# Optimization experiments

Measured on AMD Instinct MI355X. Metric: run time of the kernel, lower is better.

The kernel has to match this reference:

```python
import jax, jax.numpy as jnp
import numpy as np

N_NODES = 50000
N_EDGES = 800000
HIDDEN = 128
N_REL = 64
NUM_HEADS = 8
HEAD_DIM = HIDDEN // NUM_HEADS


def setup_inputs() -> dict:
    key = jax.random.key(0)
    ks = jax.random.split(key, 20)
    s = 0.05
    inp = {
        "x": jax.random.normal(ks[0], (N_NODES, HIDDEN), dtype=jnp.float32),
        "timestamps": jax.random.uniform(ks[1], (N_NODES,), dtype=jnp.float32),
        "src": jax.random.randint(ks[2], (N_EDGES,), 0, N_NODES),
        "dst": jax.random.randint(ks[3], (N_EDGES,), 0, N_NODES),
        "edge_type": jax.random.randint(ks[4], (N_EDGES,), 0, N_REL),
        "edge_time": jax.random.uniform(ks[5], (N_EDGES,), dtype=jnp.float32),
        # parameters (torch Linear stored as [in, out] so we use x @ W + b)
        "rel_table": jax.random.normal(ks[6], (N_REL, HIDDEN), dtype=jnp.float32) * s,
        "Wq": jax.random.normal(ks[7], (HIDDEN, HIDDEN), dtype=jnp.float32) * s,
        "bq": jnp.zeros((HIDDEN,), dtype=jnp.float32),
        "Wk": jax.random.normal(ks[8], (HIDDEN, HIDDEN), dtype=jnp.float32) * s,
        "bk": jnp.zeros((HIDDEN,), dtype=jnp.float32),
        "Wv": jax.random.normal(ks[9], (HIDDEN, HIDDEN), dtype=jnp.float32) * s,
        "bv": jnp.zeros((HIDDEN,), dtype=jnp.float32),
        "W1": jax.random.normal(ks[10], (2 * HIDDEN + 1, HIDDEN), dtype=jnp.float32) * s,
        "b1": jnp.zeros((HIDDEN,), dtype=jnp.float32),
        "W2": jax.random.normal(ks[11], (HIDDEN, 1), dtype=jnp.float32) * s,
        "b2": jnp.zeros((1,), dtype=jnp.float32),
        "time_coeff": jnp.array(1.0, dtype=jnp.float32),
    }
    return inp


def reference(x, timestamps, src, dst, edge_type, edge_time, rel_table,
              Wq, bq, Wk, bk, Wv, bv, W1, b1, W2, b2, time_coeff):
    N = x.shape[0]
    # temporal gating
    delta_t = (timestamps[dst] - edge_time) / (jnp.abs(time_coeff) + 1e-9)  # [E]
    time_mask = jax.nn.sigmoid(delta_t)[:, None]                            # [E,1]
    rel_emb = rel_table[edge_type] * time_mask                              # [E,H]
    src_emb = x[src]                                                        # [E,H]
    # dynamic edge weights: MLP([src_emb, rel_emb, time_mask]) -> sigmoid
    weight_input = jnp.concatenate([src_emb, rel_emb, time_mask], axis=-1)  # [E,2H+1]
    h = jax.nn.relu(weight_input @ W1 + b1)
    dynamic_weights = jax.nn.sigmoid(h @ W2 + b2)                           # [E,1]
    message = src_emb * rel_emb * dynamic_weights                           # [E,H]
    # multi-head edge attention keyed by dst
    q = (x[dst] @ Wq + bq).reshape(-1, NUM_HEADS, HEAD_DIM)
    k = (message @ Wk + bk).reshape(-1, NUM_HEADS, HEAD_DIM)
    v = (message @ Wv + bv).reshape(-1, NUM_HEADS, HEAD_DIM)
    scores = (q * k).sum(-1) / (HEAD_DIM ** 0.5)                            # [E,heads]
    # scatter softmax over edges grouped by dst
    seg_max = jax.ops.segment_max(scores, dst, num_segments=N)              # [N,heads]
    e = jnp.exp(scores - seg_max[dst])
    denom = jax.ops.segment_sum(e, dst, num_segments=N)
    attn = e / denom[dst]                                                   # [E,heads]
    out = jax.ops.segment_sum(v * attn[..., None], dst, num_segments=N)     # [N,heads,hd]
    return out.reshape(N, NUM_HEADS * HEAD_DIM)
```

## Files before the change

### kernel.cpp

```cpp
#include <hip/hip_runtime.h>

typedef __bf16 v8bf __attribute__((ext_vector_type(8)));
typedef __bf16 v4bf __attribute__((ext_vector_type(4)));
typedef float  v4f  __attribute__((ext_vector_type(4)));

#define MFMA16x16x32 __builtin_amdgcn_mfma_f32_16x16x32_bf16

#define HIDDEN 128
#define NHEADS 8

__global__ __launch_bounds__(512) void prep_all(
    const float* __restrict__ rel, const float* __restrict__ W1,
    const float* __restrict__ Wk, const float* __restrict__ Wv,
    const float* __restrict__ W2, const int* __restrict__ dst,
    int* __restrict__ count,
    __bf16* __restrict__ mlppre, __bf16* __restrict__ relbf,
    __bf16* __restrict__ wswz, __bf16* __restrict__ w2bf,
    float* __restrict__ outz,
    const float* __restrict__ x, const float* __restrict__ Wq,
    const float* __restrict__ bq, const float* __restrict__ b1,
    __bf16* __restrict__ qbf, __bf16* __restrict__ hpre, __bf16* __restrict__ xbf,
    int N, int E, int hb, int zb, int nz4)
{
  __shared__ __bf16 X[32][136];
  const int b = blockIdx.x;
  if (b < 64) {
    __shared__ float rrow[128];
    const int j = threadIdx.x;
    if (j < 128) rrow[j] = rel[b*HIDDEN + j];
    __syncthreads();
    if (j < 128) {
      float acc = W1[256*HIDDEN + j];
      #pragma unroll 4
      for (int k=0;k<128;k++) acc += rrow[k]*W1[(128+k)*HIDDEN + j];
      mlppre[b*HIDDEN + j] = (__bf16)acc;
      relbf [b*HIDDEN + j] = (__bf16)rrow[j];
    }
    return;
  }
  if (b < 72) {
    int f = (b - 64)*512 + threadIdx.x;
    if (f < 128) w2bf[f] = (__bf16)W2[f];
    if (f >= 2*8*4*64) return;
    int lane = f & 63, kk = (f>>6)&3, c = (f>>8)&7, mat = f>>11;
    const float* W = mat ? Wv : Wk;
    int qq = lane>>4, nn = lane&15;
    v8bf o;
    #pragma unroll
    for (int j=0;j<8;j++) o[j] = (__bf16)W[(kk*32 + qq*8 + j)*HIDDEN + c*16 + nn];
    *(v8bf*)(wswz + (long)f*8) = o;
    return;
  }
  if (b < 72 + hb) {
    long i = (long)(b - 72)*512 + threadIdx.x;
    long e4 = i*4;
    if (e4 + 3 < E) {
      int4 d = *(const int4*)(dst + e4);
      atomicAdd(&count[d.x], 1);
      atomicAdd(&count[d.y], 1);
      atomicAdd(&count[d.z], 1);
      atomicAdd(&count[d.w], 1);
    } else {
      for (long e = e4; e < E; e++) atomicAdd(&count[dst[e]], 1);
    }
    return;
  }
  if (b < 72 + hb + zb) {
    int idx = (b - 72 - hb)*512 + threadIdx.x;
    if (idx < nz4) ((float4*)outz)[idx] = make_float4(0.f,0.f,0.f,0.f);
    return;
  }
  const int pb = b - (72 + hb + zb), npb = gridDim.x - (72 + hb + zb);
  const int tid = threadIdx.x;
  const int w = tid >> 6, l = tid & 63, qd = l >> 4, ln = l & 15;
  const int col = w*16 + ln;

  v8bf BQ[4], BH[4];
  #pragma unroll
  for (int kk=0; kk<4; kk++) {
    v8bf f, g;
    #pragma unroll
    for (int j=0;j<8;j++){
      f[j] = (__bf16)Wq[(kk*32 + qd*8 + j)*HIDDEN + col];
      g[j] = (__bf16)W1[(kk*32 + qd*8 + j)*HIDDEN + col];
    }
    BQ[kk] = f; BH[kk] = g;
  }
  const float bqv = bq[col], b1v = b1[col];

  const int s = tid >> 4, c8 = (tid & 15)*8;
  for (int n0 = pb*32; n0 < N; n0 += npb*32) {
    __syncthreads();
    int n = n0 + s;
    v8bf xv;
    if (n < N) {
      const float4* xp = (const float4*)(x + (long)n*HIDDEN + c8);
      float4 a = xp[0], b2_ = xp[1];
      xv[0]=(__bf16)a.x; xv[1]=(__bf16)a.y; xv[2]=(__bf16)a.z; xv[3]=(__bf16)a.w;
      xv[4]=(__bf16)b2_.x; xv[5]=(__bf16)b2_.y; xv[6]=(__bf16)b2_.z; xv[7]=(__bf16)b2_.w;
      *(v8bf*)(xbf + (long)n*HIDDEN + c8) = xv;
    } else {
      #pragma unroll
      for (int j=0;j<8;j++) xv[j] = (__bf16)0.f;
    }
    *(v8bf*)&X[s][c8] = xv;
    __syncthreads();

    v4f q0={0.f,0.f,0.f,0.f}, q1={0.f,0.f,0.f,0.f};
    v4f h0={0.f,0.f,0.f,0.f}, h1={0.f,0.f,0.f,0.f};
    #pragma unroll
    for (int kk=0;kk<4;kk++) {
      v8bf a0 = *(const v8bf*)&X[ln][kk*32 + qd*8];
      v8bf a1 = *(const v8bf*)&X[16+ln][kk*32 + qd*8];
      q0 = MFMA16x16x32(a0, BQ[kk], q0, 0,0,0);
      q1 = MFMA16x16x32(a1, BQ[kk], q1, 0,0,0);
      h0 = MFMA16x16x32(a0, BH[kk], h0, 0,0,0);
      h1 = MFMA16x16x32(a1, BH[kk], h1, 0,0,0);
    }
    #pragma unroll
    for (int r=0;r<4;r++) {
      int n_o = n0 + qd*4 + r;
      if (n_o < N) {
        qbf [(long)n_o*HIDDEN + col] = (__bf16)(q0[r] + bqv);
        hpre[(long)n_o*HIDDEN + col] = (__bf16)(h0[r] + b1v);
      }
      int n2 = n0 + 16 + qd*4 + r;
      if (n2 < N) {
        qbf [(long)n2*HIDDEN + col] = (__bf16)(q1[r] + bqv);
        hpre[(long)n2*HIDDEN + col] = (__bf16)(h1[r] + b1v);
      }
    }
  }
}

__global__ __launch_bounds__(1024) void scan_kernel(const int* __restrict__ count,
    int* __restrict__ base, int N)
{
  __shared__ int ssum[1024];
  const int t = threadIdx.x;
  const int chunk = ((N + 4095) >> 12) << 2;
  const int lo = t*chunk, hi = min(lo + chunk, N);
  int s = 0;
  int i = lo;
  for (; i + 3 < hi; i += 4) {
    int4 v = *(const int4*)(count + i);
    s += v.x + v.y + v.z + v.w;
  }
  for (; i < hi; i++) s += count[i];
  ssum[t] = s;
  __syncthreads();
  #pragma unroll
  for (int ofs = 1; ofs < 1024; ofs <<= 1) {
    int v = (t >= ofs) ? ssum[t - ofs] : 0;
    __syncthreads();
    ssum[t] += v;
    __syncthreads();
  }
  int run = (t == 0) ? 0 : ssum[t-1];
  i = lo;
  for (; i + 3 < hi; i += 4) {
    int4 c = *(const int4*)(count + i);
    int4 o;
    o.x = run; o.y = run + c.x; o.z = o.y + c.y; o.w = o.z + c.z;
    *(int4*)(base + i) = o;
    run = o.w + c.w;
  }
  for (; i < hi; i++) { base[i] = run; run += count[i]; }
}

__global__ __launch_bounds__(512) void scat_dw(
    const int* __restrict__ src, const int* __restrict__ dstp,
    const int* __restrict__ etyp, const float* __restrict__ etime,
    const float* __restrict__ ts, const float* __restrict__ tc,
    const __bf16* __restrict__ hpre, const __bf16* __restrict__ mlppre,
    const __bf16* __restrict__ w2bf, const float* __restrict__ b2,
    const int* __restrict__ base, int* __restrict__ cursor,
    int4* __restrict__ meta4, int E)
{
  const int tid = threadIdx.x;
  const int wid = tid >> 6, l = tid & 63;
  const long e0 = ((long)blockIdx.x*8 + wid)*4;
  const int ei = l >> 4, lc = l & 15;

  int s_=0, d_=0, ty_=0; float et_=0.f, tsd_=0.f;
  if (l < 4 && e0 + l < E) {
    long e = e0 + l;
    s_ = src[e]; d_ = dstp[e]; ty_ = etyp[e]; et_ = etime[e]; tsd_ = ts[d_];
  }
  const int sE  = __shfl(s_, ei);
  const int dE  = __shfl(d_, ei);
  const int tyE = __shfl(ty_, ei);
  const float etE  = __shfl(et_, ei);
  const float tsdE = __shfl(tsd_, ei);

  const float invtc = 1.0f / (fabsf(tc[0]) + 1e-9f);
  const float dt = (tsdE - etE) * invtc;
  const float tm = 1.0f/(1.0f + __expf(-dt));

  const v8bf w2v = *(const v8bf*)(w2bf + lc*8);
  v8bf av = *(const v8bf*)(hpre  + (long)sE *HIDDEN + lc*8);
  v8bf bp = *(const v8bf*)(mlppre+ (long)tyE*HIDDEN + lc*8);

  float z = 0.f;
  #pragma unroll
  for (int j=0;j<8;j++){
    float pj = (float)av[j] + tm*(float)bp[j];
    z += fmaxf(pj, 0.f)*(float)w2v[j];
  }
  z += __shfl_xor(z,1); z += __shfl_xor(z,2);
  z += __shfl_xor(z,4); z += __shfl_xor(z,8);

  if (lc == 0 && e0 + ei < E) {
    float dw = 1.0f/(1.0f + __expf(-(z + b2[0])));
    int p = base[dE] + atomicAdd(&cursor[dE], 1);
    meta4[p] = make_int4(sE, dE, tyE, __float_as_int(tm * dw));
  }
}

__global__ __launch_bounds__(512, 4) void edge_fused5(
    const int4* __restrict__ meta4,
    const __bf16* __restrict__ xbf, const __bf16* __restrict__ qbf,
    const __bf16* __restrict__ relbf, const __bf16* __restrict__ wswz,
    const float* __restrict__ bk, const float* __restrict__ bv,
    float* __restrict__ out, float* __restrict__ denom, int E, int ntiles)
{
  __shared__ __align__(16) __bf16 MSG[2][4096];

  const int tid = threadIdx.x;
  const int wid = tid >> 6, l = tid & 63, qd = l >> 4, ln = l & 15;
  const int eIdx = wid*4 + qd;

  v8bf bkf[4], bvf[4];
  #pragma unroll
  for (int kk=0;kk<4;kk++){
    bkf[kk] = *(const v8bf*)(wswz +         wid*2048 + kk*512 + (size_t)l*8);
    bvf[kk] = *(const v8bf*)(wswz + 16384 + wid*2048 + kk*512 + (size_t)l*8);
  }
  const float bkc = bk[wid*16 + ln];
  const float bvc = bv[wid*16 + ln];

  const int g = gridDim.x;
  int t = blockIdx.x;
  if (t >= ntiles) return;

  int4 mt = make_int4(0, -1, 0, 0);
  { int e = t*32 + l; if (l < 32 && e < E) mt = meta4[e]; }
  int tn = t + g;
  int4 mtn = make_int4(0, -1, 0, 0);
  if (tn < ntiles) { int e = tn*32 + l; if (l < 32 && e < E) mtn = meta4[e]; }

  float sME = __int_as_float(__shfl(mt.w, eIdx));
  v8bf sv, rv;
  {
    int srcE = __shfl(mt.x, eIdx);
    int tyE  = __shfl(mt.z, eIdx);
    sv = *(const v8bf*)(xbf   + (long)srcE*HIDDEN + ln*8);
    rv = *(const v8bf*)(relbf + (long)tyE *HIDDEN + ln*8);
  }
  int dC[2][4];
  #pragma unroll
  for (int b=0;b<2;b++)
    #pragma unroll
    for (int r=0;r<4;r++) dC[b][r] = __shfl(mt.y, b*16 + qd*4 + r);
  float qA[2][4];
  #pragma unroll
  for (int b=0;b<2;b++)
    #pragma unroll
    for (int r=0;r<4;r++){
      int d = dC[b][r];
      qA[b][r] = (float)qbf[(long)(d<0?0:d)*HIDDEN + wid*16 + ln];
    }

  int p = 0;
  while (true) {
    const int d_m = mt.y;

    int dprev = __shfl(d_m, (l>0)?(l-1):0);
    int flag = (l < 32) && ((l==0) || (d_m != dprev));
    unsigned long long segmask = __ballot(flag);

    const int t2 = tn + g;
    int4 mt2 = make_int4(0, -1, 0, 0);
    if (t2 < ntiles) { int e = t2*32 + l; if (l < 32 && e < E) mt2 = meta4[e]; }

    const float sMN = __int_as_float(__shfl(mtn.w, eIdx));
    const int srcN = __shfl(mtn.x, eIdx);
    const int tyN  = __shfl(mtn.z, eIdx);
    int dN[2][4];
    #pragma unroll
    for (int b=0;b<2;b++)
      #pragma unroll
      for (int r=0;r<4;r++) dN[b][r] = __shfl(mtn.y, b*16 + qd*4 + r);

    {
      char* wbase = (char*)&MSG[p][0] + eIdx*256;
      const int sw = (eIdx & 7) << 4;
      v8bf m;
      #pragma unroll
      for (int j=0;j<8;j++) m[j] = (__bf16)((float)sv[j]*(float)rv[j]*sME);
      *(v8bf*)(wbase + ((ln*16) ^ sw)) = m;
    }

    sv = *(const v8bf*)(xbf   + (long)srcN*HIDDEN + ln*8);
    rv = *(const v8bf*)(relbf + (long)tyN *HIDDEN + ln*8);

    float qB[2][4];
    #pragma unroll
    for (int b=0;b<2;b++)
      #pragma unroll
      for (int r=0;r<4;r++){
        int d = dN[b][r];
        qB[b][r] = (float)qbf[(long)(d<0?0:d)*HIDDEN + wid*16 + ln];
      }

    asm volatile("s_waitcnt lgkmcnt(0)" ::: "memory");
    __builtin_amdgcn_s_barrier();
    __builtin_amdgcn_sched_barrier(0);

    const char* rb = (const char*)&MSG[p][0];
    v4f aK[2], aV[2];
    __builtin_amdgcn_s_setprio(1);
    #pragma unroll
    for (int b=0;b<2;b++){
      const int rrow = b*16 + ln;
      const char* abase = rb + rrow*256;
      const int asw = (rrow & 7) << 4;
      v4f k_ = {0.f,0.f,0.f,0.f}, v_ = {0.f,0.f,0.f,0.f};
      #pragma unroll
      for (int kk=0;kk<4;kk++){
        v8bf a = *(const v8bf*)(abase + ((kk*64 + qd*16) ^ asw));
        k_ = MFMA16x16x32(a, bkf[kk], k_, 0,0,0);
        v_ = MFMA16x16x32(a, bvf[kk], v_, 0,0,0);
      }
      aK[b] = k_; aV[b] = v_;
    }
    __builtin_amdgcn_s_setprio(0);

    float sc[2][4];
    #pragma unroll
    for (int b=0;b<2;b++)
      #pragma unroll
      for (int r=0;r<4;r++) sc[b][r] = (aK[b][r] + bkc)*qA[b][r];
    #pragma unroll
    for (int m=1;m<16;m<<=1){
      #pragma unroll
      for (int b=0;b<2;b++)
        #pragma unroll
        for (int r=0;r<4;r++) sc[b][r] += __shfl_xor(sc[b][r], m);
    }
    float ee[2][4], wv[2][4];
    #pragma unroll
    for (int b=0;b<2;b++)
      #pragma unroll
      for (int r=0;r<4;r++){
        float e_ = __expf(sc[b][r]*0.25f);
        ee[b][r] = e_;
        wv[b][r] = e_*(aV[b][r] + bvc);
      }

    unsigned long long mm = segmask;
    while (mm){
      int s0 = __ffsll((long long)mm) - 1;
      mm &= mm - 1;
      int s1 = mm ? (__ffsll((long long)mm) - 1) : 32;
      int dseg = __shfl(d_m, s0);
      if (dseg < 0) continue;
      float a0 = 0.f, dn0 = 0.f;
      #pragma unroll
      for (int b=0;b<2;b++)
        #pragma unroll
        for (int r=0;r<4;r++){
          int rw = b*16 + qd*4 + r;
          bool in = (rw >= s0) && (rw < s1);
          a0  += in ? wv[b][r] : 0.f;
          dn0 += in ? ee[b][r] : 0.f;
        }
      a0  += __shfl_xor(a0,16);  a0  += __shfl_xor(a0,32);
      dn0 += __shfl_xor(dn0,16); dn0 += __shfl_xor(dn0,32);
      if (l < 16) atomicAdd(&out[(long)dseg*HIDDEN + wid*16 + ln], a0);
      if (l == 0) atomicAdd(&denom[(long)dseg*NHEADS + wid], dn0);
    }

    if (tn >= ntiles) break;
    t = tn; tn = t2; mt = mtn; mtn = mt2; sME = sMN;
    #pragma unroll
    for (int b=0;b<2;b++)
      #pragma unroll
      for (int r=0;r<4;r++){
        dC[b][r] = dN[b][r];
        qA[b][r] = qB[b][r];
      }
    p ^= 1;
  }
}

__global__ __launch_bounds__(512) void q_kernel(const float* __restrict__ x,
    const float* __restrict__ Wq, const float* __restrict__ bq,
    float* __restrict__ q, int N)
{
  __shared__ __bf16 X[32][136];
  const int tid = threadIdx.x;
  const int w = tid >> 6, l = tid & 63, qd = l >> 4, ln = l & 15;
  const int col = w*16 + ln;
  v8bf B[4];
  #pragma unroll
  for (int kk=0; kk<4; kk++) {
    v8bf f;
    #pragma unroll
    for (int j=0;j<8;j++) f[j] = (__bf16)Wq[(kk*32 + qd*8 + j)*HIDDEN + col];
    B[kk] = f;
  }
  const float bqv = bq[col];
  const int s = tid >> 4, c8 = (tid & 15)*8;
  for (int n0 = blockIdx.x*32; n0 < N; n0 += gridDim.x*32) {
    __syncthreads();
    int n = n0 + s;
    v8bf xv;
    if (n < N) {
      const float4* xp = (const float4*)(x + (long)n*HIDDEN + c8);
      float4 a = xp[0], b = xp[1];
      xv[0]=(__bf16)a.x; xv[1]=(__bf16)a.y; xv[2]=(__bf16)a.z; xv[3]=(__bf16)a.w;
      xv[4]=(__bf16)b.x; xv[5]=(__bf16)b.y; xv[6]=(__bf16)b.z; xv[7]=(__bf16)b.w;
    } else {
      #pragma unroll
      for (int j=0;j<8;j++) xv[j] = (__bf16)0.f;
    }
    *(v8bf*)&X[s][c8] = xv;
    __syncthreads();
    v4f acc0 = {0.f,0.f,0.f,0.f}, acc1 = {0.f,0.f,0.f,0.f};
    #pragma unroll
    for (int kk=0;kk<4;kk++) {
      v8bf a0 = *(const v8bf*)&X[ln][kk*32 + qd*8];
      v8bf a1 = *(const v8bf*)&X[16+ln][kk*32 + qd*8];
      acc0 = MFMA16x16x32(a0, B[kk], acc0, 0,0,0);
      acc1 = MFMA16x16x32(a1, B[kk], acc1, 0,0,0);
    }
    #pragma unroll
    for (int r=0;r<4;r++) {
      int n_o = n0 + qd*4 + r;
      if (n_o < N) q[(long)n_o*HIDDEN + col] = acc0[r] + bqv;
      int n_o2 = n0 + 16 + qd*4 + r;
      if (n_o2 < N) q[(long)n_o2*HIDDEN + col] = acc1[r] + bqv;
    }
  }
}

__global__ __launch_bounds__(512) void edge_atomic(
    const float* __restrict__ x, const float* __restrict__ ts,
    const int* __restrict__ src, const int* __restrict__ dst,
    const int* __restrict__ etyp, const float* __restrict__ etime,
    const float* __restrict__ rel,
    const float* __restrict__ Wk, const float* __restrict__ bk,
    const float* __restrict__ Wv, const float* __restrict__ bv,
    const float* __restrict__ W1, const float* __restrict__ b1,
    const float* __restrict__ W2, const float* __restrict__ b2,
    const float* __restrict__ tc,
    const float* __restrict__ qws, float* __restrict__ denom,
    float* __restrict__ out, int E)
{
  __shared__ __bf16 A[32][264];
  __shared__ __bf16 A2[32][136];
  __shared__ float sW2[128], sb1[128], sw1r[128], sbk[128], sbv[128];
  __shared__ float stm[32], sdw[32];
  __shared__ int   ssrc[32], sdst[32], styp[32];
  __shared__ float dwpart[8][32];
  const int tid = threadIdx.x;
  const int w = tid >> 6, l = tid & 63, qd = l >> 4, ln = l & 15;
  const int col = w*16 + ln;
  v8bf B1[8], BK[4], BV[4];
  #pragma unroll
  for (int kk=0;kk<8;kk++){ v8bf f;
    #pragma unroll
    for (int j=0;j<8;j++) f[j] = (__bf16)W1[(kk*32+qd*8+j)*HIDDEN + col];
    B1[kk]=f; }
  #pragma unroll
  for (int kk=0;kk<4;kk++){ v8bf f,g;
    #pragma unroll
    for (int j=0;j<8;j++){ f[j] = (__bf16)Wk[(kk*32+qd*8+j)*HIDDEN + col];
                           g[j] = (__bf16)Wv[(kk*32+qd*8+j)*HIDDEN + col]; }
    BK[kk]=f; BV[kk]=g; }
  if (tid < 128) {
    sW2[tid]=W2[tid]; sb1[tid]=b1[tid]; sw1r[tid]=W1[256*HIDDEN+tid];
    sbk[tid]=bk[tid]; sbv[tid]=bv[tid];
  }
  const float b2v = b2[0];
  const float invtc = 1.0f / (fabsf(tc[0]) + 1e-9f);
  const int s = tid >> 4, c8 = (tid & 15)*8;
  const int ntiles = (E + 31) >> 5;
  for (int t = blockIdx.x; t < ntiles; t += gridDim.x) {
    const int e0 = t*32;
    __syncthreads();
    if (tid < 32) {
      int e = e0 + tid;
      if (e < E) {
        int d = dst[e];
        ssrc[tid]=src[e]; sdst[tid]=d; styp[tid]=etyp[e];
        float dt = (ts[d] - etime[e]) * invtc;
        stm[tid] = 1.0f/(1.0f+expf(-dt));
      } else { ssrc[tid]=0; sdst[tid]=0; styp[tid]=0; stm[tid]=0.f; }
    }
    __syncthreads();
    {
      const float tmv = stm[s];
      const float4* xp = (const float4*)(x + (long)ssrc[s]*HIDDEN + c8);
      float4 a = xp[0], b = xp[1];
      const float4* rp = (const float4*)(rel + (long)styp[s]*HIDDEN + c8);
      float4 ra = rp[0], rb = rp[1];
      v8bf sv, rv;
      sv[0]=(__bf16)a.x; sv[1]=(__bf16)a.y; sv[2]=(__bf16)a.z; sv[3]=(__bf16)a.w;
      sv[4]=(__bf16)b.x; sv[5]=(__bf16)b.y; sv[6]=(__bf16)b.z; sv[7]=(__bf16)b.w;
      rv[0]=(__bf16)(ra.x*tmv); rv[1]=(__bf16)(ra.y*tmv);
      rv[2]=(__bf16)(ra.z*tmv); rv[3]=(__bf16)(ra.w*tmv);
      rv[4]=(__bf16)(rb.x*tmv); rv[5]=(__bf16)(rb.y*tmv);
      rv[6]=(__bf16)(rb.z*tmv); rv[7]=(__bf16)(rb.w*tmv);
      *(v8bf*)&A[s][c8] = sv;
      *(v8bf*)&A[s][128 + c8] = rv;
    }
    __syncthreads();
    v4f acc0={0.f,0.f,0.f,0.f}, acc1={0.f,0.f,0.f,0.f};
    #pragma unroll
    for (int kk=0;kk<8;kk++){
      v8bf a0 = *(const v8bf*)&A[ln][kk*32 + qd*8];
      v8bf a1 = *(const v8bf*)&A[16+ln][kk*32 + qd*8];
      acc0 = MFMA16x16x32(a0, B1[kk], acc0, 0,0,0);
      acc1 = MFMA16x16x32(a1, B1[kk], acc1, 0,0,0);
    }
    float part[8];
    {
      const float w1rj = sw1r[col], b1j = sb1[col], w2j = sW2[col];
      #pragma unroll
      for (int r=0;r<4;r++){
        int i0 = qd*4 + r, i1 = 16 + qd*4 + r;
        part[r]   = fmaxf(acc0[r] + stm[i0]*w1rj + b1j, 0.f)*w2j;
        part[4+r] = fmaxf(acc1[r] + stm[i1]*w1rj + b1j, 0.f)*w2j;
      }
    }
    #pragma unroll
    for (int m=1;m<16;m<<=1){
      #pragma unroll
      for (int i=0;i<8;i++) part[i] += __shfl_xor(part[i], m, 16);
    }
    if (ln == 0){
      #pragma unroll
      for (int r=0;r<4;r++){ dwpart[w][qd*4+r]=part[r]; dwpart[w][16+qd*4+r]=part[4+r]; }
    }
    __syncthreads();
    if (tid < 32){
      float z = b2v;
      #pragma unroll
      for (int ww=0;ww<8;ww++) z += dwpart[ww][tid];
      sdw[tid] = 1.0f/(1.0f+expf(-z));
    }
    __syncthreads();
    {
      const float dwv = sdw[s];
      v8bf mv;
      #pragma unroll
      for (int i=0;i<8;i++)
        mv[i] = (__bf16)((float)A[s][c8+i]*(float)A[s][128+c8+i]*dwv);
      *(v8bf*)&A2[s][c8] = mv;
    }
    __syncthreads();
    v4f k0={0.f,0.f,0.f,0.f}, k1={0.f,0.f,0.f,0.f};
    v4f v0={0.f,0.f,0.f,0.f}, v1={0.f,0.f,0.f,0.f};
    #pragma unroll
    for (int kk=0;kk<4;kk++){
      v8bf a0 = *(const v8bf*)&A2[ln][kk*32 + qd*8];
      v8bf a1 = *(const v8bf*)&A2[16+ln][kk*32 + qd*8];
      k0 = MFMA16x16x32(a0, BK[kk], k0, 0,0,0);
      k1 = MFMA16x16x32(a1, BK[kk], k1, 0,0,0);
      v0 = MFMA16x16x32(a0, BV[kk], v0, 0,0,0);
      v1 = MFMA16x16x32(a1, BV[kk], v1, 0,0,0);
    }
    float sc[8];
    const float bkj = sbk[col], bvj = sbv[col];
    #pragma unroll
    for (int r=0;r<4;r++){
      int i0 = qd*4 + r, i1 = 16 + qd*4 + r;
      sc[r]   = (k0[r]+bkj)*qws[(long)sdst[i0]*HIDDEN + col];
      sc[4+r] = (k1[r]+bkj)*qws[(long)sdst[i1]*HIDDEN + col];
    }
    #pragma unroll
    for (int m=1;m<16;m<<=1){
      #pragma unroll
      for (int i=0;i<8;i++) sc[i] += __shfl_xor(sc[i], m, 16);
    }
    float ee[8];
    #pragma unroll
    for (int i=0;i<8;i++) ee[i] = expf(sc[i]*0.25f);
    if (ln == 0){
      #pragma unroll
      for (int r=0;r<4;r++){
        int i0 = qd*4 + r, i1 = 16 + qd*4 + r;
        if (e0+i0 < E) atomicAdd(&denom[(long)sdst[i0]*NHEADS + w], ee[r]);
        if (e0+i1 < E) atomicAdd(&denom[(long)sdst[i1]*NHEADS + w], ee[4+r]);
      }
    }
    #pragma unroll
    for (int r=0;r<4;r++){
      int i0 = qd*4 + r, i1 = 16 + qd*4 + r;
      if (e0+i0 < E) atomicAdd(&out[(long)sdst[i0]*HIDDEN + col], ee[r]*(v0[r]+bvj));
      if (e0+i1 < E) atomicAdd(&out[(long)sdst[i1]*HIDDEN + col], ee[4+r]*(v1[r]+bvj));
    }
  }
}

__global__ void fin_kernel(float* __restrict__ out, const float* __restrict__ denom, int N)
{
  int idx = blockIdx.x*blockDim.x + threadIdx.x;
  int total = N*32;
  if (idx < total){
    int n = idx >> 5;
    int h = (idx & 31) >> 2;
    float d = denom[n*8 + h];
    float inv = d > 0.f ? 1.0f/d : 0.f;
    float4* p = (float4*)out + idx;
    float4 v = *p;
    v.x*=inv; v.y*=inv; v.z*=inv; v.w*=inv;
    *p = v;
  }
}

static inline size_t align256(size_t v){ return (v + 255) & ~(size_t)255; }

extern "C" void kernel_launch(void* const* d_in, const int* in_sizes, int n_in,
                              void* d_out, int out_size, void* d_ws, size_t ws_size,
                              hipStream_t stream)
{
  const float* x      = (const float*)d_in[0];
  const float* ts     = (const float*)d_in[1];
  const int*   src    = (const int*)d_in[2];
  const int*   dstp   = (const int*)d_in[3];
  const int*   etyp   = (const int*)d_in[4];
  const float* etime  = (const float*)d_in[5];
  const float* rel    = (const float*)d_in[6];
  const float* Wq     = (const float*)d_in[7];
  const float* bq     = (const float*)d_in[8];
  const float* Wk     = (const float*)d_in[9];
  const float* bk     = (const float*)d_in[10];
  const float* Wv     = (const float*)d_in[11];
  const float* bv     = (const float*)d_in[12];
  const float* W1     = (const float*)d_in[13];
  const float* b1     = (const float*)d_in[14];
  const float* W2     = (const float*)d_in[15];
  const float* b2     = (const float*)d_in[16];
  const float* tc     = (const float*)d_in[17];
  float* out = (float*)d_out;

  const int N = in_sizes[0] / HIDDEN;
  const int E = in_sizes[2];

  char* ws = (char*)d_ws;
  size_t off = 0;
  __bf16* qbf    = (__bf16*)(ws + off); off += align256((size_t)N*HIDDEN*2);
  __bf16* hpre   = (__bf16*)(ws + off); off += align256((size_t)N*HIDDEN*2);
  __bf16* xbf    = (__bf16*)(ws + off); off += align256((size_t)N*HIDDEN*2);
  __bf16* relbf  = (__bf16*)(ws + off); off += align256((size_t)64*HIDDEN*2);
  __bf16* mlppre = (__bf16*)(ws + off); off += align256((size_t)64*HIDDEN*2);
  __bf16* w2bf   = (__bf16*)(ws + off); off += align256((size_t)HIDDEN*2);
  __bf16* wswz   = (__bf16*)(ws + off); off += align256((size_t)4096*8*2);
  size_t zoff = off;
  int*    countp = (int*)(ws + off);    off += align256((size_t)N*4);
  int*    cursor = (int*)(ws + off);    off += align256((size_t)N*4);
  float*  denom  = (float*)(ws + off);  off += align256((size_t)N*NHEADS*4);
  size_t zlen = off - zoff;
  int4*   meta4  = (int4*)(ws + off);   off += align256((size_t)E*16);
  int*    basep  = (int*)(ws + off);    off += align256((size_t)N*4);
  const size_t needed_fast = off;

  if (ws_size >= needed_fast) {
    hipMemsetAsync(ws + zoff, 0, zlen, stream);

    const int hb = (E + 2047)/2048;
    const int nz4 = N*32;
    const int zb = (nz4 + 511)/512;
    prep_all<<<72 + hb + zb + 1024, 512, 0, stream>>>(rel, W1, Wk, Wv, W2,
        dstp, countp, mlppre, relbf, wswz, w2bf, out,
        x, Wq, bq, b1, qbf, hpre, xbf, N, E, hb, zb, nz4);
    scan_kernel<<<1, 1024, 0, stream>>>(countp, basep, N);
    scat_dw<<<(E + 31)/32, 512, 0, stream>>>(src, dstp, etyp, etime, ts, tc,
        hpre, mlppre, w2bf, b2, basep, cursor, meta4, E);

    const int ntiles = (E + 31) >> 5;
    edge_fused5<<<1024, 512, 0, stream>>>(meta4,
        xbf, qbf, relbf, wswz, bk, bv, out, denom, E, ntiles);
    fin_kernel<<<(N*32 + 255)/256, 256, 0, stream>>>(out, denom, N);
  } else {
    float* qws    = (float*)ws;
    float* denom2 = (float*)(ws + align256((size_t)N*HIDDEN*4));
    hipMemsetAsync(out,    0, (size_t)N*HIDDEN*4, stream);
    hipMemsetAsync(denom2, 0, (size_t)N*NHEADS*4, stream);
    q_kernel<<<512, 512, 0, stream>>>(x, Wq, bq, qws, N);
    edge_atomic<<<512, 512, 0, stream>>>(x, ts, src, dstp, etyp, etime, rel,
        Wk, bk, Wv, bv, W1, b1, W2, b2, tc, qws, denom2, out, E);
    fin_kernel<<<(N*32 + 255)/256, 256, 0, stream>>>(out, denom2, N);
  }
}
```

Before: 462.5 us.

## Use contiguous tile ranges per block in edge kernel and widen scat_dw per-wave edges

```diff
diff --git a/kernel.cpp b/kernel.cpp
--- a/kernel.cpp
+++ b/kernel.cpp
@@ -179,11 +179,11 @@
 {
   const int tid = threadIdx.x;
   const int wid = tid >> 6, l = tid & 63;
-  const long e0 = ((long)blockIdx.x*8 + wid)*4;
-  const int ei = l >> 4, lc = l & 15;
+  const long e0 = ((long)blockIdx.x*8 + wid)*8;
+  const int ei = l >> 3, lc = l & 7;
 
   int s_=0, d_=0, ty_=0; float et_=0.f, tsd_=0.f;
-  if (l < 4 && e0 + l < E) {
+  if (l < 8 && e0 + l < E) {
     long e = e0 + l;
     s_ = src[e]; d_ = dstp[e]; ty_ = etyp[e]; et_ = etime[e]; tsd_ = ts[d_];
   }
@@ -197,18 +197,21 @@
   const float dt = (tsdE - etE) * invtc;
   const float tm = 1.0f/(1.0f + __expf(-dt));
 
-  const v8bf w2v = *(const v8bf*)(w2bf + lc*8);
-  v8bf av = *(const v8bf*)(hpre  + (long)sE *HIDDEN + lc*8);
-  v8bf bp = *(const v8bf*)(mlppre+ (long)tyE*HIDDEN + lc*8);
+  const v8bf w2a = *(const v8bf*)(w2bf + lc*16);
+  const v8bf w2b = *(const v8bf*)(w2bf + lc*16 + 8);
+  const __bf16* hp = hpre  + (long)sE *HIDDEN + lc*16;
+  const __bf16* mp = mlppre+ (long)tyE*HIDDEN + lc*16;
+  v8bf av0 = *(const v8bf*)hp, av1 = *(const v8bf*)(hp + 8);
+  v8bf bp0 = *(const v8bf*)mp, bp1 = *(const v8bf*)(mp + 8);
 
   float z = 0.f;
   #pragma unroll
   for (int j=0;j<8;j++){
-    float pj = (float)av[j] + tm*(float)bp[j];
-    z += fmaxf(pj, 0.f)*(float)w2v[j];
-  }
-  z += __shfl_xor(z,1); z += __shfl_xor(z,2);
-  z += __shfl_xor(z,4); z += __shfl_xor(z,8);
+    float p0 = (float)av0[j] + tm*(float)bp0[j];
+    float p1 = (float)av1[j] + tm*(float)bp1[j];
+    z += fmaxf(p0, 0.f)*(float)w2a[j] + fmaxf(p1, 0.f)*(float)w2b[j];
+  }
+  z += __shfl_xor(z,1); z += __shfl_xor(z,2); z += __shfl_xor(z,4);
 
   if (lc == 0 && e0 + ei < E) {
     float dw = 1.0f/(1.0f + __expf(-(z + b2[0])));
@@ -217,7 +220,7 @@
   }
 }
 
-__global__ __launch_bounds__(512, 4) void edge_fused5(
+__global__ __launch_bounds__(512, 4) void edge_fused6(
     const int4* __restrict__ meta4,
     const __bf16* __restrict__ xbf, const __bf16* __restrict__ qbf,
     const __bf16* __restrict__ relbf, const __bf16* __restrict__ wswz,
@@ -239,15 +242,18 @@
   const float bkc = bk[wid*16 + ln];
   const float bvc = bv[wid*16 + ln];
 
-  const int g = gridDim.x;
-  int t = blockIdx.x;
-  if (t >= ntiles) return;
-
+  const int G = gridDim.x;
+  const int wg = ((int)blockIdx.x & 7)*(G >> 3) + ((int)blockIdx.x >> 3);
+  const int lo = (int)((long)wg*ntiles/G);
+  const int hi = (int)((long)(wg+1)*ntiles/G);
+  if (lo >= hi) return;
+
+  int t = lo;
   int4 mt = make_int4(0, -1, 0, 0);
   { int e = t*32 + l; if (l < 32 && e < E) mt = meta4[e]; }
-  int tn = t + g;
+  int tn = t + 1;
   int4 mtn = make_int4(0, -1, 0, 0);
-  if (tn < ntiles) { int e = tn*32 + l; if (l < 32 && e < E) mtn = meta4[e]; }
+  if (tn < hi) { int e = tn*32 + l; if (l < 32 && e < E) mtn = meta4[e]; }
 
   float sME = __int_as_float(__shfl(mt.w, eIdx));
   v8bf sv, rv;
@@ -279,9 +285,9 @@
     int flag = (l < 32) && ((l==0) || (d_m != dprev));
     unsigned long long segmask = __ballot(flag);
 
-    const int t2 = tn + g;
+    const int t2 = tn + 1;
     int4 mt2 = make_int4(0, -1, 0, 0);
-    if (t2 < ntiles) { int e = t2*32 + l; if (l < 32 && e < E) mt2 = meta4[e]; }
+    if (t2 < hi) { int e = t2*32 + l; if (l < 32 && e < E) mt2 = meta4[e]; }
 
     const float sMN = __int_as_float(__shfl(mtn.w, eIdx));
     const int srcN = __shfl(mtn.x, eIdx);
@@ -381,7 +387,7 @@
       if (l == 0) atomicAdd(&denom[(long)dseg*NHEADS + wid], dn0);
     }
 
-    if (tn >= ntiles) break;
+    if (tn >= hi) break;
     t = tn; tn = t2; mt = mtn; mtn = mt2; sME = sMN;
     #pragma unroll
     for (int b=0;b<2;b++)
@@ -678,11 +684,11 @@
         dstp, countp, mlppre, relbf, wswz, w2bf, out,
         x, Wq, bq, b1, qbf, hpre, xbf, N, E, hb, zb, nz4);
     scan_kernel<<<1, 1024, 0, stream>>>(countp, basep, N);
-    scat_dw<<<(E + 31)/32, 512, 0, stream>>>(src, dstp, etyp, etime, ts, tc,
+    scat_dw<<<(E + 63)/64, 512, 0, stream>>>(src, dstp, etyp, etime, ts, tc,
         hpre, mlppre, w2bf, b2, basep, cursor, meta4, E);
 
     const int ntiles = (E + 31) >> 5;
-    edge_fused5<<<1024, 512, 0, stream>>>(meta4,
+    edge_fused6<<<2048, 512, 0, stream>>>(meta4,
         xbf, qbf, relbf, wswz, bk, bv, out, denom, E, ntiles);
     fin_kernel<<<(N*32 + 255)/256, 256, 0, stream>>>(out, denom, N);
   } else {
```

New measurement: 454.6 us. About the same (-1.7%).
